# Optimization experiments

Measured on AMD Instinct MI355X. Metric: run time of the kernel, lower is better.

The kernel has to match this reference:

```python
import jax, jax.numpy as jnp
import numpy as np

ALPHA, BETA, THRESH, T_SIM = 0.9, 0.8, 1.0, 10

@jax.custom_vjp
def spike(x):
    # Heaviside forward, SuperSpike surrogate gradient in backward
    return (x > 0).astype(x.dtype)

def _spike_fwd(x):
    return (x > 0).astype(x.dtype), x

def _spike_bwd(x, g):
    return (g / (100.0 * jnp.abs(x) + 1.0) ** 2,)

spike.defvjp(_spike_fwd, _spike_bwd)

def _conv_relu(x, w, b, stride):
    y = jax.lax.conv_general_dilated(x, w, (stride, stride), 'VALID',
                                     dimension_numbers=('NCHW', 'OIHW', 'NCHW'))
    return jax.nn.relu(y + b[None, :, None, None])

def setup_inputs() -> dict:
    key = jax.random.key(0)
    ks = jax.random.split(key, 16)
    B = 256
    FC_IN = 64 * 24 * 24 + 90  # conv out (24x24x64) + history 90 = 36954
    def p(k, shape, fan_in):
        return (jax.random.normal(k, shape, jnp.float32) / np.sqrt(fan_in)).astype(jnp.float32)
    return {
        'state':   jax.random.normal(ks[0], (B, 3, 224, 224), jnp.float32),
        'history': jax.random.normal(ks[1], (B, 90), jnp.float32),
        'conv1_w': p(ks[2], (32, 3, 8, 8), 3 * 8 * 8),
        'conv1_b': jnp.zeros((32,), jnp.float32),
        'conv2_w': p(ks[3], (64, 32, 4, 4), 32 * 4 * 4),
        'conv2_b': jnp.zeros((64,), jnp.float32),
        'conv3_w': p(ks[4], (64, 64, 3, 3), 64 * 3 * 3),
        'conv3_b': jnp.zeros((64,), jnp.float32),
        'fc1_w': p(ks[5], (128, FC_IN), FC_IN),
        'fc1_b': jnp.zeros((128,), jnp.float32),
        'fc2_w': p(ks[6], (256, 128), 128),
        'fc2_b': jnp.zeros((256,), jnp.float32),
        'fc3_w': p(ks[7], (9, 256), 256),
        'fc3_b': jnp.zeros((9,), jnp.float32),
    }

def reference(state, history, conv1_w, conv1_b, conv2_w, conv2_b, conv3_w, conv3_b,
              fc1_w, fc1_b, fc2_w, fc2_b, fc3_w, fc3_b):
    B = state.shape[0]
    x = _conv_relu(state, conv1_w, conv1_b, 4)   # [B,32,55,55]
    x = _conv_relu(x, conv2_w, conv2_b, 2)       # [B,64,26,26]
    x = _conv_relu(x, conv3_w, conv3_b, 1)       # [B,64,24,24]
    feats = x.reshape(B, -1)
    base = jnp.concatenate([feats, history], axis=1)
    h1 = base @ fc1_w.T + fc1_b  # loop-invariant (fc1 of a fixed input)

    def neuron(h, mem, syn):
        syn = ALPHA * syn + h
        mem = BETA * mem + syn
        out = spike(mem - THRESH)
        return out, mem - out * THRESH, syn

    z1 = jnp.zeros((B, 128), state.dtype)
    z2 = jnp.zeros((B, 256), state.dtype)
    z3 = jnp.zeros((B, 9), state.dtype)

    def step(carry, _):
        mem1, syn1, mem2, syn2, mem3, syn3, pot = carry
        spk1, mem1, syn1 = neuron(h1, mem1, syn1)
        h2 = spk1 @ fc2_w.T + fc2_b
        spk2, mem2, syn2 = neuron(h2, mem2, syn2)
        h3 = spk2 @ fc3_w.T + fc3_b
        syn3 = ALPHA * syn3 + h3
        mem3 = BETA * mem3 + syn3
        return (mem1, syn1, mem2, syn2, mem3, syn3, pot + mem3), None

    carry, _ = jax.lax.scan(step, (z1, z1, z2, z2, z3, z3, z3), None, length=T_SIM)
    return carry[6] / T_SIM
```

## Files before the change

### kernel.cpp

```cpp
#include <hip/hip_runtime.h>
#include <cstddef>
#include <cstdint>

#define ALPHA 0.9f
#define BETA  0.8f

#define FEAT   36864
#define HIST   90
#define K1     36954
#define KP     36960

typedef __attribute__((ext_vector_type(8))) short short8;
typedef __attribute__((ext_vector_type(4))) float f32x4;
typedef __attribute__((ext_vector_type(2))) int int2v;

__device__ __forceinline__ unsigned short f2bf(float x) {
  unsigned u = __float_as_uint(x);
  return (unsigned short)((u + 0x7FFFu + ((u >> 16) & 1u)) >> 16);
}
__device__ __forceinline__ float bf2f(unsigned short h) {
  return __uint_as_float(((unsigned)h) << 16);
}

__device__ __forceinline__ short8 cvt_hi_lo8(const float* __restrict__ v, short8& lov) {
  union { unsigned u[4]; short8 s; } H, L;
#pragma unroll
  for (int q = 0; q < 4; ++q) {
    unsigned h, l;
    asm("v_cvt_pk_bf16_f32 %0, %1, %2" : "=v"(h) : "v"(v[2 * q]), "v"(v[2 * q + 1]));
    float h0 = __uint_as_float(h << 16);
    float h1 = __uint_as_float(h & 0xffff0000u);
    asm("v_cvt_pk_bf16_f32 %0, %1, %2" : "=v"(l) : "v"(v[2 * q] - h0), "v"(v[2 * q + 1] - h1));
    H.u[q] = h; L.u[q] = l;
  }
  lov = L.s;
  return H.s;
}

__device__ __forceinline__ void cvt2(float v0, float v1, unsigned& hp, unsigned& lp) {
  asm("v_cvt_pk_bf16_f32 %0, %1, %2" : "=v"(hp) : "v"(v0), "v"(v1));
  float h0 = __uint_as_float(hp << 16);
  float h1 = __uint_as_float(hp & 0xffff0000u);
  asm("v_cvt_pk_bf16_f32 %0, %1, %2" : "=v"(lp) : "v"(v0 - h0), "v"(v1 - h1));
}

__global__ __launch_bounds__(256) void convert_w1c(const float* __restrict__ w,
    unsigned short* __restrict__ hi, unsigned short* __restrict__ lo)
{
  int i = blockIdx.x * 256 + threadIdx.x;
  if (i >= 6144) return;
  int kw = i & 7, rest = i >> 3;
  int cout = rest & 31, pair = rest >> 5;
  int c = pair >> 3, kh = pair & 7;
  float x = w[((cout * 3 + c) * 8 + kh) * 8 + kw];
  unsigned short h = f2bf(x);
  hi[i] = h; lo[i] = f2bf(x - bf2f(h));
}

__global__ __launch_bounds__(256) void conv1_mfma(const float* __restrict__ state,
    const unsigned short* __restrict__ whi, const unsigned short* __restrict__ wlo,
    const float* __restrict__ bias, unsigned short* __restrict__ ohi,
    unsigned short* __restrict__ olo, int batch0)
{
  int wv = threadIdx.x >> 6, lane = threadIdx.x & 63;
  int b = blockIdx.y;
  int l15 = lane & 15, kg = lane >> 4;
  int posbase = blockIdx.x * 192 + wv * 48;
  int rowb[3];
#pragma unroll
  for (int i = 0; i < 3; ++i) {
    int pos = posbase + i * 16 + l15;
    int cp = pos > 3024 ? 3024 : pos;
    int y = cp / 55, x = cp % 55;
    rowb[i] = (y * 4) * 224 + x * 4;
  }
  const float* ip = state + (size_t)(batch0 + b) * 150528;
  f32x4 acc[3][2];
#pragma unroll
  for (int i = 0; i < 3; ++i) {
    acc[i][0] = (f32x4){0.f, 0.f, 0.f, 0.f};
    acc[i][1] = (f32x4){0.f, 0.f, 0.f, 0.f};
  }
#pragma unroll 2
  for (int s = 0; s < 6; ++s) {
    int pair = s * 4 + kg;
    int c = pair >> 3, kh = pair & 7;
    int aoff = c * 50176 + kh * 224;
    short8 Ah[3], Al[3], Bh[2], Bl[2];
#pragma unroll
    for (int i = 0; i < 3; ++i) {
      const float* p = ip + aoff + rowb[i];
      const float4 f0 = *(const float4*)p;
      const float4 f1 = *(const float4*)(p + 4);
      float v[8] = {f0.x, f0.y, f0.z, f0.w, f1.x, f1.y, f1.z, f1.w};
      Ah[i] = cvt_hi_lo8(v, Al[i]);
    }
    int wb = (pair * 32 + l15) * 8;
#pragma unroll
    for (int nt = 0; nt < 2; ++nt) {
      Bh[nt] = *(const short8*)(whi + wb + nt * 128);
      Bl[nt] = *(const short8*)(wlo + wb + nt * 128);
    }
#pragma unroll
    for (int i = 0; i < 3; ++i)
#pragma unroll
      for (int nt = 0; nt < 2; ++nt) {
        acc[i][nt] = __builtin_amdgcn_mfma_f32_16x16x32_bf16(Ah[i], Bh[nt], acc[i][nt], 0, 0, 0);
        acc[i][nt] = __builtin_amdgcn_mfma_f32_16x16x32_bf16(Ah[i], Bl[nt], acc[i][nt], 0, 0, 0);
        acc[i][nt] = __builtin_amdgcn_mfma_f32_16x16x32_bf16(Al[i], Bh[nt], acc[i][nt], 0, 0, 0);
        acc[i][nt] = __builtin_amdgcn_mfma_f32_16x16x32_bf16(Al[i], Bl[nt], acc[i][nt], 0, 0, 0);
      }
  }
  float bv0 = bias[l15], bv1 = bias[16 + l15];
#pragma unroll
  for (int i = 0; i < 3; ++i) {
#pragma unroll
    for (int r = 0; r < 4; ++r) {
      int pos = posbase + i * 16 + kg * 4 + r;
      if (pos < 3025) {
        size_t o = ((size_t)b * 3025 + pos) * 32 + l15;
        float v0 = acc[i][0][r] + bv0; v0 = v0 > 0.f ? v0 : 0.f;
        float v1 = acc[i][1][r] + bv1; v1 = v1 > 0.f ? v1 : 0.f;
        unsigned hp, lp;
        cvt2(v0, v1, hp, lp);
        ohi[o]      = (unsigned short)(hp & 0xffff);
        ohi[o + 16] = (unsigned short)(hp >> 16);
        olo[o]      = (unsigned short)(lp & 0xffff);
        olo[o + 16] = (unsigned short)(lp >> 16);
      }
    }
  }
}

__global__ __launch_bounds__(256) void convert_w2(const float* __restrict__ w,
    unsigned short* __restrict__ hi, unsigned short* __restrict__ lo)
{
  int i = blockIdx.x * 256 + threadIdx.x;
  if (i >= 16 * 64 * 32) return;
  int tap = i >> 11, rem = i & 2047;
  int co = rem >> 5, ci = rem & 31;
  float x = w[co * 512 + ci * 16 + tap];
  unsigned short h = f2bf(x);
  hi[i] = h; lo[i] = f2bf(x - bf2f(h));
}

__global__ __launch_bounds__(256) void conv2_mfma(const unsigned short* __restrict__ xhi,
    const unsigned short* __restrict__ xlo, const unsigned short* __restrict__ whi,
    const unsigned short* __restrict__ wlo, const float* __restrict__ bias,
    unsigned short* __restrict__ ohi, unsigned short* __restrict__ olo, int batch0)
{
  int wv = threadIdx.x >> 6, lane = threadIdx.x & 63;
  int b0 = blockIdx.y * 2;
  int l15 = lane & 15, kg = lane >> 4;
  int posbase = blockIdx.x * 192 + wv * 48;
  int pv[3];
#pragma unroll
  for (int i = 0; i < 3; ++i) {
    int pos = posbase + i * 16 + l15;
    int cp = pos > 675 ? 675 : pos;
    int y = cp / 26, x = cp % 26;
    pv[i] = (2 * y) * 55 + 2 * x;
  }
  size_t ibase0 = (size_t)b0 * 96800;
  size_t ibase1 = ibase0 + 96800;
  int ibn[4];
#pragma unroll
  for (int nt = 0; nt < 4; ++nt) ibn[nt] = (nt * 16 + l15) * 32 + kg * 8;
  f32x4 acc[2][3][4];
#pragma unroll
  for (int bb = 0; bb < 2; ++bb)
#pragma unroll
    for (int i = 0; i < 3; ++i)
#pragma unroll
      for (int nt = 0; nt < 4; ++nt) acc[bb][i][nt] = (f32x4){0.f, 0.f, 0.f, 0.f};

#pragma unroll 2
  for (int tap = 0; tap < 16; ++tap) {
    int kh = tap >> 2, kw = tap & 3;
    int wb = tap * 2048;
    short8 A0h[3], A0l[3], A1h[3], A1l[3], Bh[4], Bl[4];
#pragma unroll
    for (int i = 0; i < 3; ++i) {
      int ia = (pv[i] + kh * 55 + kw) * 32 + kg * 8;
      A0h[i] = *(const short8*)(xhi + ibase0 + ia);
      A0l[i] = *(const short8*)(xlo + ibase0 + ia);
      A1h[i] = *(const short8*)(xhi + ibase1 + ia);
      A1l[i] = *(const short8*)(xlo + ibase1 + ia);
    }
#pragma unroll
    for (int nt = 0; nt < 4; ++nt) {
      Bh[nt] = *(const short8*)(whi + wb + ibn[nt]);
      Bl[nt] = *(const short8*)(wlo + wb + ibn[nt]);
    }
#pragma unroll
    for (int i = 0; i < 3; ++i)
#pragma unroll
      for (int nt = 0; nt < 4; ++nt) {
        acc[0][i][nt] = __builtin_amdgcn_mfma_f32_16x16x32_bf16(A0h[i], Bh[nt], acc[0][i][nt], 0, 0, 0);
        acc[0][i][nt] = __builtin_amdgcn_mfma_f32_16x16x32_bf16(A0h[i], Bl[nt], acc[0][i][nt], 0, 0, 0);
        acc[0][i][nt] = __builtin_amdgcn_mfma_f32_16x16x32_bf16(A0l[i], Bh[nt], acc[0][i][nt], 0, 0, 0);
        acc[1][i][nt] = __builtin_amdgcn_mfma_f32_16x16x32_bf16(A1h[i], Bh[nt], acc[1][i][nt], 0, 0, 0);
        acc[1][i][nt] = __builtin_amdgcn_mfma_f32_16x16x32_bf16(A1h[i], Bl[nt], acc[1][i][nt], 0, 0, 0);
        acc[1][i][nt] = __builtin_amdgcn_mfma_f32_16x16x32_bf16(A1l[i], Bh[nt], acc[1][i][nt], 0, 0, 0);
      }
  }
  float bv[4];
#pragma unroll
  for (int nt = 0; nt < 4; ++nt) bv[nt] = bias[nt * 16 + l15];
#pragma unroll
  for (int bb = 0; bb < 2; ++bb) {
    size_t obase = (size_t)(batch0 + b0 + bb) * 676;
#pragma unroll
    for (int i = 0; i < 3; ++i) {
#pragma unroll
      for (int r = 0; r < 4; ++r) {
        int pos = posbase + i * 16 + kg * 4 + r;
        if (pos < 676) {
          size_t o = (obase + pos) * 64 + l15;
#pragma unroll
          for (int np = 0; np < 2; ++np) {
            float v0 = acc[bb][i][2 * np][r] + bv[2 * np];         v0 = v0 > 0.f ? v0 : 0.f;
            float v1 = acc[bb][i][2 * np + 1][r] + bv[2 * np + 1]; v1 = v1 > 0.f ? v1 : 0.f;
            unsigned hp, lp;
            cvt2(v0, v1, hp, lp);
            ohi[o + (2 * np) * 16]     = (unsigned short)(hp & 0xffff);
            ohi[o + (2 * np + 1) * 16] = (unsigned short)(hp >> 16);
            olo[o + (2 * np) * 16]     = (unsigned short)(lp & 0xffff);
            olo[o + (2 * np + 1) * 16] = (unsigned short)(lp >> 16);
          }
        }
      }
    }
  }
}

__global__ __launch_bounds__(256) void convert_w3(const float* __restrict__ w,
    unsigned short* __restrict__ hi, unsigned short* __restrict__ lo)
{
  int i = blockIdx.x * 256 + threadIdx.x;
  if (i >= 9 * 64 * 64) return;
  int tap = i >> 12, rem = i & 4095;
  int cout = rem >> 6, cin = rem & 63;
  float x = w[cout * 576 + cin * 9 + tap];
  unsigned short h = f2bf(x);
  hi[i] = h; lo[i] = f2bf(x - bf2f(h));
}

__global__ __launch_bounds__(256) void conv3_mfma(const unsigned short* __restrict__ xhi,
    const unsigned short* __restrict__ xlo, const unsigned short* __restrict__ whi,
    const unsigned short* __restrict__ wlo, const float* __restrict__ bias,
    unsigned short* __restrict__ bhi, unsigned short* __restrict__ blo)
{
  __shared__ unsigned short slabh[260 * 40];
  __shared__ unsigned short slabl[260 * 40];
  int t = threadIdx.x;
  int wv = t >> 6, lane = t & 63;
  int pchunk = blockIdx.x;
  int b = blockIdx.y;
  const unsigned short* gh = xhi + (size_t)b * 43264 + pchunk * 13312;
  const unsigned short* gl = xlo + (size_t)b * 43264 + pchunk * 13312;
  int l15 = lane & 15, kg = lane >> 4;
  int posbase = pchunk * 192 + wv * 48;
  int lr[3], lx[3];
#pragma unroll
  for (int i = 0; i < 3; ++i) {
    int pos = posbase + i * 16 + l15;
    int y = pos / 24, x = pos % 24;
    lr[i] = y - pchunk * 8;
    lx[i] = x;
  }
  int ibn[4];
#pragma unroll
  for (int nt = 0; nt < 4; ++nt) ibn[nt] = (nt * 16 + l15) * 64 + kg * 8;
  f32x4 acc[3][4];
#pragma unroll
  for (int i = 0; i < 3; ++i)
#pragma unroll
    for (int nt = 0; nt < 4; ++nt) acc[i][nt] = (f32x4){0.f, 0.f, 0.f, 0.f};

#pragma unroll 1
  for (int ks = 0; ks < 2; ++ks) {
    if (ks) __syncthreads();
    for (int e = t; e < 1040; e += 256) {
      int p = e >> 2, s = e & 3;
      *(short8*)(slabh + p * 40 + s * 8) = *(const short8*)(gh + p * 64 + ks * 32 + s * 8);
      *(short8*)(slabl + p * 40 + s * 8) = *(const short8*)(gl + p * 64 + ks * 32 + s * 8);
    }
    __syncthreads();
    int ko = ks * 32;
#pragma unroll 3
    for (int tap = 0; tap < 9; ++tap) {
      int kh = tap / 3, kw = tap % 3;
      int wboff = tap * 4096 + ko;
      short8 Ah[3], Al[3], Bh[4], Bl[4];
#pragma unroll
      for (int i = 0; i < 3; ++i) {
        int p = (lr[i] + kh) * 26 + lx[i] + kw;
        int d = p * 40 + kg * 8;
        Ah[i] = *(const short8*)(slabh + d);
        Al[i] = *(const short8*)(slabl + d);
      }
#pragma unroll
      for (int nt = 0; nt < 4; ++nt) {
        Bh[nt] = *(const short8*)(whi + wboff + ibn[nt]);
        Bl[nt] = *(const short8*)(wlo + wboff + ibn[nt]);
      }
#pragma unroll
      for (int i = 0; i < 3; ++i)
#pragma unroll
        for (int nt = 0; nt < 4; ++nt) {
          acc[i][nt] = __builtin_amdgcn_mfma_f32_16x16x32_bf16(Ah[i], Bh[nt], acc[i][nt], 0, 0, 0);
          acc[i][nt] = __builtin_amdgcn_mfma_f32_16x16x32_bf16(Ah[i], Bl[nt], acc[i][nt], 0, 0, 0);
          acc[i][nt] = __builtin_amdgcn_mfma_f32_16x16x32_bf16(Al[i], Bh[nt], acc[i][nt], 0, 0, 0);
        }
    }
  }
  float bv[4];
#pragma unroll
  for (int nt = 0; nt < 4; ++nt) bv[nt] = bias[nt * 16 + l15];
  size_t ob = (size_t)b * KP;
#pragma unroll
  for (int i = 0; i < 3; ++i) {
#pragma unroll
    for (int r = 0; r < 4; ++r) {
      int pos = posbase + i * 16 + kg * 4 + r;
      size_t o = ob + (size_t)pos * 64 + l15;
#pragma unroll
      for (int np = 0; np < 2; ++np) {
        float v0 = acc[2 * np][0][r];
        v0 = acc[i][2 * np][r] + bv[2 * np];               v0 = v0 > 0.f ? v0 : 0.f;
        float v1 = acc[i][2 * np + 1][r] + bv[2 * np + 1]; v1 = v1 > 0.f ? v1 : 0.f;
        unsigned hp, lp;
        cvt2(v0, v1, hp, lp);
        bhi[o + (2 * np) * 16]     = (unsigned short)(hp & 0xffff);
        bhi[o + (2 * np + 1) * 16] = (unsigned short)(hp >> 16);
        blo[o + (2 * np) * 16]     = (unsigned short)(lp & 0xffff);
        blo[o + (2 * np + 1) * 16] = (unsigned short)(lp >> 16);
      }
    }
  }
}

__global__ __launch_bounds__(128) void fill_hist(const float* __restrict__ hist,
    unsigned short* __restrict__ bhi, unsigned short* __restrict__ blo)
{
  int b = blockIdx.x, t = threadIdx.x;
  int k = FEAT + t;
  if (k >= KP) return;
  float x = (k < K1) ? hist[b * HIST + t] : 0.f;
  unsigned short h = f2bf(x);
  size_t o = (size_t)b * KP + k;
  bhi[o] = h; blo[o] = f2bf(x - bf2f(h));
}

__global__ __launch_bounds__(256) void convert_w1(const float* __restrict__ w,
    unsigned short* __restrict__ hi, unsigned short* __restrict__ lo)
{
  __shared__ float tl[64][65];
  int o = blockIdx.y;
  int p0 = blockIdx.x * 64;
  int t = threadIdx.x;
  const float* src = w + (size_t)o * K1;
  for (int e = t; e < 4096; e += 256) {
    int c = e >> 6, p = e & 63;
    tl[p][c] = src[c * 576 + p0 + p];
  }
  __syncthreads();
  size_t dbase = (size_t)o * KP;
  for (int e = t; e < 4096; e += 256) {
    int p = e >> 6, c = e & 63;
    float x = tl[p][c];
    unsigned short h = f2bf(x);
    size_t d = dbase + (size_t)(p0 + p) * 64 + c;
    hi[d] = h; lo[d] = f2bf(x - bf2f(h));
  }
}

__global__ __launch_bounds__(128) void convert_w1_tail(const float* __restrict__ w,
    unsigned short* __restrict__ hi, unsigned short* __restrict__ lo)
{
  int o = blockIdx.x, t = threadIdx.x;
  int k = FEAT + t;
  if (k >= KP) return;
  float x = (k < K1) ? w[(size_t)o * K1 + k] : 0.f;
  unsigned short h = f2bf(x);
  size_t p = (size_t)o * KP + k;
  hi[p] = h; lo[p] = f2bf(x - bf2f(h));
}

__global__ __launch_bounds__(256) void transpose_fc2(const float* __restrict__ w,
                                                     float* __restrict__ wT)
{
  int idx = blockIdx.x * 256 + threadIdx.x;
  if (idx < 128 * 256) {
    int i = idx >> 8, j = idx & 255;
    wT[idx] = w[j * 128 + i];
  }
}

__global__ __launch_bounds__(256) void fc1_mfma(const unsigned short* __restrict__ bhi,
    const unsigned short* __restrict__ blo, const unsigned short* __restrict__ whi,
    const unsigned short* __restrict__ wlo, float* __restrict__ part)
{
  int w = threadIdx.x >> 6, lane = threadIdx.x & 63;
  int job = blockIdx.x * 4 + w;
  int mt2 = job & 7, nt = job >> 3;
  int ks = blockIdx.y;
  int k0 = ks * 35 * 32;
  int l15 = lane & 15, kg = lane >> 4;
  int s0 = mt2 * 32 + l15;
  int o  = nt * 16 + l15;
  const unsigned short* pa0h = bhi + (size_t)s0 * KP + k0 + kg * 8;
  const unsigned short* pa1h = pa0h + (size_t)16 * KP;
  const unsigned short* pa0l = blo + (size_t)s0 * KP + k0 + kg * 8;
  const unsigned short* pa1l = pa0l + (size_t)16 * KP;
  const unsigned short* pbh  = whi + (size_t)o * KP + k0 + kg * 8;
  const unsigned short* pbl  = wlo + (size_t)o * KP + k0 + kg * 8;
  f32x4 acc0 = {0.f, 0.f, 0.f, 0.f}, acc1 = {0.f, 0.f, 0.f, 0.f};
#pragma unroll 1
  for (int i = 0; i < 35; ++i) {
    short8 a0h = *(const short8*)pa0h;
    short8 a1h = *(const short8*)pa1h;
    short8 a0l = *(const short8*)pa0l;
    short8 a1l = *(const short8*)pa1l;
    short8 bh  = *(const short8*)pbh;
    short8 bl  = *(const short8*)pbl;
    acc0 = __builtin_amdgcn_mfma_f32_16x16x32_bf16(a0h, bh, acc0, 0, 0, 0);
    acc1 = __builtin_amdgcn_mfma_f32_16x16x32_bf16(a1h, bh, acc1, 0, 0, 0);
    acc0 = __builtin_amdgcn_mfma_f32_16x16x32_bf16(a0h, bl, acc0, 0, 0, 0);
    acc1 = __builtin_amdgcn_mfma_f32_16x16x32_bf16(a1h, bl, acc1, 0, 0, 0);
    acc0 = __builtin_amdgcn_mfma_f32_16x16x32_bf16(a0l, bh, acc0, 0, 0, 0);
    acc1 = __builtin_amdgcn_mfma_f32_16x16x32_bf16(a1l, bh, acc1, 0, 0, 0);
    pa0h += 32; pa1h += 32; pa0l += 32; pa1l += 32; pbh += 32; pbl += 32;
  }
  float* pp0 = part + (((size_t)ks * 64 + job) * 2) * 256;
  float* pp1 = pp0 + 256;
#pragma unroll
  for (int r = 0; r < 4; ++r) {
    pp0[r * 64 + lane] = acc0[r];
    pp1[r * 64 + lane] = acc1[r];
  }
}

__global__ __launch_bounds__(256) void fc1_reduce(const float* __restrict__ part,
                                                  float* __restrict__ h1)
{
  int i = blockIdx.x * 256 + threadIdx.x;
  if (i >= 32768) return;
  int s = i >> 7, o = i & 127;
  int mt2 = s >> 5, ti = (s >> 4) & 1, nt = o >> 4;
  int job = nt * 8 + mt2;
  int r = s & 15, c = o & 15;
  int off = (job * 2 + ti) * 256 + (r & 3) * 64 + ((r >> 2) << 4) + c;
  float sum = 0.f;
#pragma unroll 1
  for (int ks = 0; ks < 33; ++ks) sum += part[(size_t)ks * 32768 + off];
  h1[i] = sum;
}

__global__ __launch_bounds__(256) void snn_ker(const float* __restrict__ h1,
    const float* __restrict__ b1, const float* __restrict__ w2T,
    const float* __restrict__ b2p, const float* __restrict__ w3,
    const float* __restrict__ b3p, float* __restrict__ out)
{
  int b = blockIdx.x, t = threadIdx.x;
  __shared__ float spk1l[128];
  __shared__ float part[4][9];
  float h1v = 0.f;
  if (t < 128) h1v = h1[b * 128 + t] + b1[t];
  float b2 = b2p[t];
  float w3r[9];
#pragma unroll
  for (int j = 0; j < 9; ++j) w3r[j] = w3[j * 256 + t];
  float mem1 = 0.f, syn1 = 0.f, mem2 = 0.f, syn2 = 0.f;
  float syn3[9], mem3[9], pot[9];
#pragma unroll
  for (int j = 0; j < 9; ++j) { syn3[j] = 0.f; mem3[j] = 0.f; pot[j] = 0.f; }

#pragma unroll 1
  for (int step = 0; step < 10; ++step) {
    if (t < 128) {
      syn1 = ALPHA * syn1 + h1v;
      mem1 = BETA * mem1 + syn1;
      float s = (mem1 > 1.0f) ? 1.f : 0.f;
      spk1l[t] = s;
      mem1 -= s;
    }
    __syncthreads();
    float h2 = b2;
#pragma unroll
    for (int i = 0; i < 128; ++i) {
      h2 += spk1l[i] * w2T[i * 256 + t];
    }
    syn2 = ALPHA * syn2 + h2;
    mem2 = BETA * mem2 + syn2;
    float s2 = (mem2 > 1.0f) ? 1.f : 0.f;
    mem2 -= s2;

    float v[9];
#pragma unroll
    for (int j = 0; j < 9; ++j) v[j] = s2 * w3r[j];
#pragma unroll
    for (int j = 0; j < 9; ++j) {
      v[j] += __shfl_down(v[j], 32);
      v[j] += __shfl_down(v[j], 16);
      v[j] += __shfl_down(v[j], 8);
      v[j] += __shfl_down(v[j], 4);
      v[j] += __shfl_down(v[j], 2);
      v[j] += __shfl_down(v[j], 1);
    }
    if ((t & 63) == 0) {
#pragma unroll
      for (int j = 0; j < 9; ++j) part[t >> 6][j] = v[j];
    }
    __syncthreads();
    if (t == 0) {
#pragma unroll
      for (int j = 0; j < 9; ++j) {
        float h3 = part[0][j] + part[1][j] + part[2][j] + part[3][j] + b3p[j];
        syn3[j] = ALPHA * syn3[j] + h3;
        mem3[j] = BETA * mem3[j] + syn3[j];
        pot[j] += mem3[j];
      }
    }
  }
  if (t == 0) {
#pragma unroll
    for (int j = 0; j < 9; ++j) out[b * 9 + j] = pot[j] / 10.0f;
  }
}

extern "C" void kernel_launch(void* const* d_in, const int* in_sizes, int n_in,
                              void* d_out, int out_size, void* d_ws, size_t ws_size,
                              hipStream_t stream)
{
  const float* state = (const float*)d_in[0];
  const float* hist  = (const float*)d_in[1];
  const float* c1w   = (const float*)d_in[2];
  const float* c1b   = (const float*)d_in[3];
  const float* c2w   = (const float*)d_in[4];
  const float* c2b   = (const float*)d_in[5];
  const float* c3w   = (const float*)d_in[6];
  const float* c3b   = (const float*)d_in[7];
  const float* f1w   = (const float*)d_in[8];
  const float* f1b   = (const float*)d_in[9];
  const float* f2w   = (const float*)d_in[10];
  const float* f2b   = (const float*)d_in[11];
  const float* f3w   = (const float*)d_in[12];
  const float* f3b   = (const float*)d_in[13];
  float* out = (float*)d_out;
  float* ws  = (float*)d_ws;

  unsigned short* c1hi    = (unsigned short*)(ws);
  unsigned short* c1lo    = (unsigned short*)(ws + 6195200);
  unsigned short* base_hi = (unsigned short*)(ws);
  unsigned short* base_lo = (unsigned short*)(ws + 4730880);
  unsigned short* c2hi    = (unsigned short*)(ws + 12390400);
  unsigned short* c2lo    = (unsigned short*)(ws + 17928192);
  unsigned short* w1_hi   = (unsigned short*)(ws + 23465984);
  unsigned short* w1_lo   = (unsigned short*)(ws + 25831424);
  float* partb    = ws + 28196864;
  unsigned short* w1chi   = (unsigned short*)(ws + 29278208);
  unsigned short* w1clo   = (unsigned short*)(ws + 29281280);
  unsigned short* w2_hi   = (unsigned short*)(ws + 29284352);
  unsigned short* w2_lo   = (unsigned short*)(ws + 29300736);
  unsigned short* w3_hi   = (unsigned short*)(ws + 29317120);
  unsigned short* w3_lo   = (unsigned short*)(ws + 29335552);
  float* h1buf    = ws + 29353984;
  float* wT2      = ws + 29386752;

  convert_w1c<<<dim3(24), 256, 0, stream>>>(c1w, w1chi, w1clo);
  convert_w2<<<dim3(128), 256, 0, stream>>>(c2w, w2_hi, w2_lo);
  convert_w3<<<dim3(144), 256, 0, stream>>>(c3w, w3_hi, w3_lo);
  for (int p = 0; p < 2; ++p) {
    conv1_mfma<<<dim3(16, 128), 256, 0, stream>>>(state, w1chi, w1clo, c1b,
                                                  c1hi, c1lo, p * 128);
    conv2_mfma<<<dim3(4, 64), 256, 0, stream>>>(c1hi, c1lo, w2_hi, w2_lo, c2b,
                                                c2hi, c2lo, p * 128);
  }
  convert_w1<<<dim3(9, 128), 256, 0, stream>>>(f1w, w1_hi, w1_lo);
  convert_w1_tail<<<dim3(128), 128, 0, stream>>>(f1w, w1_hi, w1_lo);
  fill_hist<<<dim3(256), 128, 0, stream>>>(hist, base_hi, base_lo);
  conv3_mfma<<<dim3(3, 256), 256, 0, stream>>>(c2hi, c2lo, w3_hi, w3_lo, c3b,
                                               base_hi, base_lo);
  transpose_fc2<<<dim3(128), 256, 0, stream>>>(f2w, wT2);
  fc1_mfma<<<dim3(16, 33), 256, 0, stream>>>(base_hi, base_lo, w1_hi, w1_lo, partb);
  fc1_reduce<<<dim3(128), 256, 0, stream>>>(partb, h1buf);
  snn_ker<<<dim3(256), 256, 0, stream>>>(h1buf, f1b, wT2, f2b, f3w, f3b, out);
}
```

Before: 353.0 us.

## Enlarge fc1 MFMA wave tile to 32x32 for operand reuse

The fc1 split-K GEMM now has each wave compute a 32x32 output tile (two M by two N sub-tiles) instead of 32x16. The same A and B fragments feed more MFMAs, which cuts global loads per MFMA, and the grid shrinks from 16x33 to 8x33 blocks. The partial-sum layout and the reduce kernel's indexing change to match. A dead load in the conv3 epilogue is also removed. The trade-off is fewer waves to hide memory latency and more accumulator registers per wave.

```diff
diff --git a/kernel.cpp b/kernel.cpp
--- a/kernel.cpp
+++ b/kernel.cpp
@@ -327,8 +327,7 @@
       size_t o = ob + (size_t)pos * 64 + l15;
 #pragma unroll
       for (int np = 0; np < 2; ++np) {
-        float v0 = acc[2 * np][0][r];
-        v0 = acc[i][2 * np][r] + bv[2 * np];               v0 = v0 > 0.f ? v0 : 0.f;
+        float v0 = acc[i][2 * np][r] + bv[2 * np];         v0 = v0 > 0.f ? v0 : 0.f;
         float v1 = acc[i][2 * np + 1][r] + bv[2 * np + 1]; v1 = v1 > 0.f ? v1 : 0.f;
         unsigned hp, lp;
         cvt2(v0, v1, hp, lp);
@@ -404,42 +403,58 @@
 {
   int w = threadIdx.x >> 6, lane = threadIdx.x & 63;
   int job = blockIdx.x * 4 + w;
-  int mt2 = job & 7, nt = job >> 3;
+  int mt2 = job >> 2, nt2 = job & 3;
   int ks = blockIdx.y;
   int k0 = ks * 35 * 32;
   int l15 = lane & 15, kg = lane >> 4;
   int s0 = mt2 * 32 + l15;
-  int o  = nt * 16 + l15;
+  int o0 = nt2 * 32 + l15;
   const unsigned short* pa0h = bhi + (size_t)s0 * KP + k0 + kg * 8;
   const unsigned short* pa1h = pa0h + (size_t)16 * KP;
   const unsigned short* pa0l = blo + (size_t)s0 * KP + k0 + kg * 8;
   const unsigned short* pa1l = pa0l + (size_t)16 * KP;
-  const unsigned short* pbh  = whi + (size_t)o * KP + k0 + kg * 8;
-  const unsigned short* pbl  = wlo + (size_t)o * KP + k0 + kg * 8;
-  f32x4 acc0 = {0.f, 0.f, 0.f, 0.f}, acc1 = {0.f, 0.f, 0.f, 0.f};
+  const unsigned short* pb0h = whi + (size_t)o0 * KP + k0 + kg * 8;
+  const unsigned short* pb1h = pb0h + (size_t)16 * KP;
+  const unsigned short* pb0l = wlo + (size_t)o0 * KP + k0 + kg * 8;
+  const unsigned short* pb1l = pb0l + (size_t)16 * KP;
+  f32x4 acc[2][2];
+  acc[0][0] = (f32x4){0.f, 0.f, 0.f, 0.f};
+  acc[0][1] = (f32x4){0.f, 0.f, 0.f, 0.f};
+  acc[1][0] = (f32x4){0.f, 0.f, 0.f, 0.f};
+  acc[1][1] = (f32x4){0.f, 0.f, 0.f, 0.f};
 #pragma unroll 1
   for (int i = 0; i < 35; ++i) {
     short8 a0h = *(const short8*)pa0h;
     short8 a1h = *(const short8*)pa1h;
     short8 a0l = *(const short8*)pa0l;
     short8 a1l = *(const short8*)pa1l;
-    short8 bh  = *(const short8*)pbh;
-    short8 bl  = *(const short8*)pbl;
-    acc0 = __builtin_amdgcn_mfma_f32_16x16x32_bf16(a0h, bh, acc0, 0, 0, 0);
-    acc1 = __builtin_amdgcn_mfma_f32_16x16x32_bf16(a1h, bh, acc1, 0, 0, 0);
-    acc0 = __builtin_amdgcn_mfma_f32_16x16x32_bf16(a0h, bl, acc0, 0, 0, 0);
-    acc1 = __builtin_amdgcn_mfma_f32_16x16x32_bf16(a1h, bl, acc1, 0, 0, 0);
-    acc0 = __builtin_amdgcn_mfma_f32_16x16x32_bf16(a0l, bh, acc0, 0, 0, 0);
-    acc1 = __builtin_amdgcn_mfma_f32_16x16x32_bf16(a1l, bh, acc1, 0, 0, 0);
-    pa0h += 32; pa1h += 32; pa0l += 32; pa1l += 32; pbh += 32; pbl += 32;
-  }
-  float* pp0 = part + (((size_t)ks * 64 + job) * 2) * 256;
-  float* pp1 = pp0 + 256;
-#pragma unroll
-  for (int r = 0; r < 4; ++r) {
-    pp0[r * 64 + lane] = acc0[r];
-    pp1[r * 64 + lane] = acc1[r];
-  }
+    short8 b0h = *(const short8*)pb0h;
+    short8 b1h = *(const short8*)pb1h;
+    short8 b0l = *(const short8*)pb0l;
+    short8 b1l = *(const short8*)pb1l;
+    acc[0][0] = __builtin_amdgcn_mfma_f32_16x16x32_bf16(a0h, b0h, acc[0][0], 0, 0, 0);
+    acc[0][1] = __builtin_amdgcn_mfma_f32_16x16x32_bf16(a0h, b1h, acc[0][1], 0, 0, 0);
+    acc[1][0] = __builtin_amdgcn_mfma_f32_16x16x32_bf16(a1h, b0h, acc[1][0], 0, 0, 0);
+    acc[1][1] = __builtin_amdgcn_mfma_f32_16x16x32_bf16(a1h, b1h, acc[1][1], 0, 0, 0);
+    acc[0][0] = __builtin_amdgcn_mfma_f32_16x16x32_bf16(a0h, b0l, acc[0][0], 0, 0, 0);
+    acc[0][1] = __builtin_amdgcn_mfma_f32_16x16x32_bf16(a0h, b1l, acc[0][1], 0, 0, 0);
+    acc[1][0] = __builtin_amdgcn_mfma_f32_16x16x32_bf16(a1h, b0l, acc[1][0], 0, 0, 0);
+    acc[1][1] = __builtin_amdgcn_mfma_f32_16x16x32_bf16(a1h, b1l, acc[1][1], 0, 0, 0);
+    acc[0][0] = __builtin_amdgcn_mfma_f32_16x16x32_bf16(a0l, b0h, acc[0][0], 0, 0, 0);
+    acc[0][1] = __builtin_amdgcn_mfma_f32_16x16x32_bf16(a0l, b1h, acc[0][1], 0, 0, 0);
+    acc[1][0] = __builtin_amdgcn_mfma_f32_16x16x32_bf16(a1l, b0h, acc[1][0], 0, 0, 0);
+    acc[1][1] = __builtin_amdgcn_mfma_f32_16x16x32_bf16(a1l, b1h, acc[1][1], 0, 0, 0);
+    pa0h += 32; pa1h += 32; pa0l += 32; pa1l += 32;
+    pb0h += 32; pb1h += 32; pb0l += 32; pb1l += 32;
+  }
+  float* pp = part + ((size_t)ks * 32 + job) * 1024;
+#pragma unroll
+  for (int mi = 0; mi < 2; ++mi)
+#pragma unroll
+    for (int ni = 0; ni < 2; ++ni)
+#pragma unroll
+      for (int r = 0; r < 4; ++r)
+        pp[(mi * 2 + ni) * 256 + r * 64 + lane] = acc[mi][ni][r];
 }
 
 __global__ __launch_bounds__(256) void fc1_reduce(const float* __restrict__ part,
@@ -448,10 +463,10 @@
   int i = blockIdx.x * 256 + threadIdx.x;
   if (i >= 32768) return;
   int s = i >> 7, o = i & 127;
-  int mt2 = s >> 5, ti = (s >> 4) & 1, nt = o >> 4;
-  int job = nt * 8 + mt2;
-  int r = s & 15, c = o & 15;
-  int off = (job * 2 + ti) * 256 + (r & 3) * 64 + ((r >> 2) << 4) + c;
+  int mt2 = s >> 5, st = s & 31, mi = st >> 4, sr = st & 15;
+  int nt2 = o >> 5, ot = o & 31, ni = ot >> 4, c = ot & 15;
+  int job = mt2 * 4 + nt2;
+  int off = (job * 4 + mi * 2 + ni) * 256 + (sr & 3) * 64 + ((sr >> 2) << 4) + c;
   float sum = 0.f;
 #pragma unroll 1
   for (int ks = 0; ks < 33; ++ks) sum += part[(size_t)ks * 32768 + off];
@@ -584,7 +599,7 @@
   conv3_mfma<<<dim3(3, 256), 256, 0, stream>>>(c2hi, c2lo, w3_hi, w3_lo, c3b,
                                                base_hi, base_lo);
   transpose_fc2<<<dim3(128), 256, 0, stream>>>(f2w, wT2);
-  fc1_mfma<<<dim3(16, 33), 256, 0, stream>>>(base_hi, base_lo, w1_hi, w1_lo, partb);
+  fc1_mfma<<<dim3(8, 33), 256, 0, stream>>>(base_hi, base_lo, w1_hi, w1_lo, partb);
   fc1_reduce<<<dim3(128), 256, 0, stream>>>(partb, h1buf);
   snn_ker<<<dim3(256), 256, 0, stream>>>(h1buf, f1b, wT2, f2b, f3w, f3b, out);
 }
```

After: 357.1 us. About the same (+1.2%).
